# Performance work log

Hardware: AMD Instinct MI355X
Metric: run time of the kernel (lower is better)

Reference implementation:

```python
import jax, jax.numpy as jnp
import numpy as np
from jax import lax

EMBED_DIM = 512
HIDDEN_DIM = 256
OUT_DIM = HIDDEN_DIM // 2
BATCH = 32
SEQ = 4096
THRESHOLD = 1.0
DECAY = 0.95
REFRACTORY = 2.0


def setup_inputs() -> dict:
    key = jax.random.key(0)
    k1, k2, k3 = jax.random.split(key, 3)
    x = jax.random.normal(k1, (BATCH, SEQ, EMBED_DIM), dtype=jnp.float32)
    input_weights = jax.random.normal(k2, (EMBED_DIM, HIDDEN_DIM), dtype=jnp.float32) * 0.1
    hidden_weights = jax.random.normal(k3, (HIDDEN_DIM, OUT_DIM), dtype=jnp.float32) * 0.1
    return {"x": x, "input_weights": input_weights, "hidden_weights": hidden_weights}


def reference(x, input_weights, hidden_weights):
    B, S, D = x.shape
    H = input_weights.shape[1]
    dt = x.dtype
    # batch-mean then project all timesteps at once: [S, H]
    currents = jnp.einsum('sd,dh->sh', x.mean(0), input_weights)

    def step(carry, ic):
        mem, refr = carry
        active = (refr <= 0).astype(dt)
        mem = DECAY * mem + ic * active
        spikes = (mem >= THRESHOLD).astype(dt)
        mem = mem * (1.0 - spikes)
        refr = jnp.maximum(refr - 1.0, 0.0) + spikes * REFRACTORY
        return (mem, refr), spikes

    init = (jnp.zeros((H,), dt), jnp.zeros((H,), dt))
    _, spikes = lax.scan(step, init, currents)  # spikes: [S, H]
    out = spikes @ hidden_weights               # [S, OUT]
    out_mean = out.mean(0)                      # mean over timesteps
    # original repeats the (batch-independent) output across the batch
    return jnp.broadcast_to(out_mean, (B, out_mean.shape[0]))
```

## Files before the change

kernel.cpp:

```cpp
#include <hip/hip_runtime.h>
#include <stdint.h>


#define S_LEN 4096
#define D_DIM 512
#define H_DIM 256
#define O_DIM 128
#define B_SZ  32

#define NPROD 512
#define NCONS 4
#define FPB   2
#define CH    64
#define NCH   (S_LEN / CH)
#define ROWS  (CH / 4)
#define FLAG_GOAL 16u

typedef const __attribute__((address_space(1))) void  glob_void;
typedef       __attribute__((address_space(3))) void  lds_void;

#define LIF_STEP(IC) {                          \
    float ict = sp2 ? 0.f : (IC);               \
    float tt  = fmaf(0.95f, u, ict);            \
    u   = sp1 ? 0.f : tt;                       \
    bool sp = (u >= 1.0f);                      \
    cnt += sp ? 1 : 0;                          \
    sp2 = sp1; sp1 = sp; }

#define ACC4(A, V) { A.x += V.x; A.y += V.y; A.z += V.z; A.w += V.w; }

__global__ __launch_bounds__(256, 2)
void snn_fused(const float4* __restrict__ x4,
               const float*  __restrict__ iw,
               const float*  __restrict__ hw,
               float4*       __restrict__ cur4,
               uint32_t*     __restrict__ flags,
               float*        __restrict__ out) {
    __shared__ __attribute__((aligned(16))) char smem[2 * ROWS * 64 * 16 + 256];
    const int t = threadIdx.x;

    if (blockIdx.x < NPROD) {
        float4* xm = (float4*)smem;
        const int r2 = t >> 7;
        const int d4 = t & 127;
        const int h  = t;
        const float inv = 1.0f / (float)B_SZ;
        const size_t bstr = (size_t)S_LEN * (D_DIM / 4);

        for (int g = 0; g < FPB; ++g) {
            const int f  = blockIdx.x + NPROD * g;
            const int s0 = 4 * f;

            float4 a0 = make_float4(0.f, 0.f, 0.f, 0.f);
            float4 a1 = make_float4(0.f, 0.f, 0.f, 0.f);
            const float4* xb = x4 + (size_t)(s0 + r2) * (D_DIM / 4) + d4;
            for (int b = 0; b < B_SZ; b += 4) {
                const float4* p = xb + (size_t)b * bstr;
                float4 v00 = p[0],            v01 = p[2 * (D_DIM / 4)];
                float4 v10 = p[bstr],         v11 = p[bstr + 2 * (D_DIM / 4)];
                float4 v20 = p[2 * bstr],     v21 = p[2 * bstr + 2 * (D_DIM / 4)];
                float4 v30 = p[3 * bstr],     v31 = p[3 * bstr + 2 * (D_DIM / 4)];
                ACC4(a0, v00); ACC4(a0, v10); ACC4(a0, v20); ACC4(a0, v30);
                ACC4(a1, v01); ACC4(a1, v11); ACC4(a1, v21); ACC4(a1, v31);
            }
            a0.x *= inv; a0.y *= inv; a0.z *= inv; a0.w *= inv;
            a1.x *= inv; a1.y *= inv; a1.z *= inv; a1.w *= inv;
            xm[r2 * (D_DIM / 4) + d4]       = a0;
            xm[(r2 + 2) * (D_DIM / 4) + d4] = a1;
            __syncthreads();

            float acc2[4] = {0.f, 0.f, 0.f, 0.f};
            for (int d4i = 0; d4i < D_DIM / 4; ++d4i) {
                const int d = d4i * 4;
                float w0 = iw[(d + 0) * H_DIM + h];
                float w1 = iw[(d + 1) * H_DIM + h];
                float w2 = iw[(d + 2) * H_DIM + h];
                float w3 = iw[(d + 3) * H_DIM + h];
                #pragma unroll
                for (int r = 0; r < 4; ++r) {
                    float4 xv = xm[r * (D_DIM / 4) + d4i];
                    acc2[r] += xv.x * w0 + xv.y * w1 + xv.z * w2 + xv.w * w3;
                }
            }
            cur4[(size_t)f * H_DIM + h] =
                make_float4(acc2[0], acc2[1], acc2[2], acc2[3]);

            __syncthreads();
            if (t == 0) {
                __builtin_amdgcn_fence(__ATOMIC_RELEASE, "agent");
                atomicAdd(&flags[f >> 4], 1u);
            }
        }
        return;
    }

    if (t >= 64) return;
    float4 (*lbuf)[ROWS * 64] = (float4 (*)[ROWS * 64])smem;
    float* cl = (float*)(smem + 2 * ROWS * 64 * 16);
    const int lane  = t;
    const int hbase = (int)(blockIdx.x - NPROD) * 64;

    auto wait_chunk = [&](int c) {
        if (lane == 0) {
            while (atomicAdd(&flags[c], 0u) < FLAG_GOAL)
                __builtin_amdgcn_s_sleep(2);
        }
        __builtin_amdgcn_fence(__ATOMIC_ACQUIRE, "agent");
    };
    auto stage = [&](int c) {
        #pragma unroll
        for (int r = 0; r < ROWS; ++r) {
            const float4* g = cur4 + (size_t)(c * ROWS + r) * H_DIM + hbase + lane;
            __builtin_amdgcn_global_load_lds((glob_void*)g,
                                             (lds_void*)&lbuf[c & 1][r * 64 + lane],
                                             16, 0, 0);
        }
    };

    wait_chunk(0);
    stage(0);

    float u = 0.f;
    int   cnt = 0;
    bool  sp1 = false, sp2 = false;

    for (int c = 0; c < NCH; ++c) {
        if (c + 1 < NCH) {
            wait_chunk(c + 1);
            stage(c + 1);
            asm volatile("s_waitcnt vmcnt(16)" ::: "memory");
        } else {
            asm volatile("s_waitcnt vmcnt(0)" ::: "memory");
        }
        const float4* lb = lbuf[c & 1];
        float4 v[ROWS];
        #pragma unroll
        for (int r = 0; r < ROWS; ++r) v[r] = lb[r * 64 + lane];
        __builtin_amdgcn_sched_barrier(0);

        #pragma unroll
        for (int r = 0; r < ROWS; ++r) {
            LIF_STEP(v[r].x); LIF_STEP(v[r].y); LIF_STEP(v[r].z); LIF_STEP(v[r].w);
        }
    }

    __syncthreads();
    cl[lane] = (float)cnt;
    __syncthreads();
    float a0 = 0.f, a1 = 0.f;
    #pragma unroll 8
    for (int k = 0; k < 64; ++k) {
        float c = cl[k];
        const float* w = hw + (size_t)(hbase + k) * O_DIM;
        a0 = fmaf(c, w[lane], a0);
        a1 = fmaf(c, w[lane + 64], a1);
    }
    a0 *= (1.0f / (float)S_LEN);
    a1 *= (1.0f / (float)S_LEN);
    for (int b = 0; b < B_SZ; ++b) {
        atomicAdd(out + b * O_DIM + lane,      a0);
        atomicAdd(out + b * O_DIM + lane + 64, a1);
    }
}

extern "C" void kernel_launch(void* const* d_in, const int* in_sizes, int n_in,
                              void* d_out, int out_size, void* d_ws, size_t ws_size,
                              hipStream_t stream) {
    const float4* x4 = (const float4*)d_in[0];
    const float*  iw = (const float*) d_in[1];
    const float*  hw = (const float*) d_in[2];
    float* out   = (float*)d_out;
    float4* cur4 = (float4*)d_ws;
    uint32_t* flags = (uint32_t*)((char*)d_ws + (size_t)4 * 1024 * 1024);

    hipMemsetAsync(flags, 0, NCH * sizeof(uint32_t), stream);
    hipMemsetAsync(out,   0, B_SZ * O_DIM * sizeof(float), stream);
    hipLaunchKernelGGL(snn_fused, dim3(NPROD + NCONS), dim3(256), 0, stream,
                       x4, iw, hw, cur4, flags, out);
}
```

Before: 496.3 us.

## Restructure producer/consumer handoff with per-pass counters and register-buffered scan

Halves the producer grid to 256 blocks, each handling 4 row-groups, and replaces the per-chunk flags with one counter per pass that consumers poll until all producers have finished that pass. Producers write currents row-major with relaxed agent-scope atomic stores. Consumers read them with relaxed atomic loads straight into two 64-float register buffers, double-buffered, instead of staging through LDS with global_load_lds. This cuts flag traffic and LDS round trips on the serial scan, but consumers now wait for a full producer pass before starting, and the acquire fences are gone, which weakens the memory-ordering guarantees.

```diff
diff --git a/kernel.cpp b/kernel.cpp
--- a/kernel.cpp
+++ b/kernel.cpp
@@ -8,16 +8,11 @@
 #define O_DIM 128
 #define B_SZ  32
 
-#define NPROD 512
+#define NPROD 256
 #define NCONS 4
-#define FPB   2
+#define FPB   4
 #define CH    64
 #define NCH   (S_LEN / CH)
-#define ROWS  (CH / 4)
-#define FLAG_GOAL 16u
-
-typedef const __attribute__((address_space(1))) void  glob_void;
-typedef       __attribute__((address_space(3))) void  lds_void;
 
 #define LIF_STEP(IC) {                          \
     float ict = sp2 ? 0.f : (IC);               \
@@ -29,14 +24,28 @@
 
 #define ACC4(A, V) { A.x += V.x; A.y += V.y; A.z += V.z; A.w += V.w; }
 
+#define CISSUE(BUF, C) {                                                     \
+    const float* p_ = csrc + (size_t)(C) * (CH * H_DIM);                     \
+    _Pragma("unroll")                                                        \
+    for (int r_ = 0; r_ < CH; ++r_)                                          \
+        BUF[r_] = __hip_atomic_load(p_ + (size_t)r_ * H_DIM,                 \
+                                    __ATOMIC_RELAXED,                        \
+                                    __HIP_MEMORY_SCOPE_AGENT);              \
+    __builtin_amdgcn_sched_barrier(0); }
+
+#define CSCAN(BUF) {                                                         \
+    _Pragma("unroll")                                                        \
+    for (int r_ = 0; r_ < CH; ++r_) { LIF_STEP(BUF[r_]); }                   \
+    __builtin_amdgcn_sched_barrier(0); }
+
 __global__ __launch_bounds__(256, 2)
 void snn_fused(const float4* __restrict__ x4,
                const float*  __restrict__ iw,
                const float*  __restrict__ hw,
-               float4*       __restrict__ cur4,
-               uint32_t*     __restrict__ flags,
+               float*        __restrict__ cur,
+               uint32_t*     __restrict__ ctr,
                float*        __restrict__ out) {
-    __shared__ __attribute__((aligned(16))) char smem[2 * ROWS * 64 * 16 + 256];
+    __shared__ __attribute__((aligned(16))) char smem[4 * 128 * 16 + 256];
     const int t = threadIdx.x;
 
     if (blockIdx.x < NPROD) {
@@ -82,66 +91,50 @@
                     acc2[r] += xv.x * w0 + xv.y * w1 + xv.z * w2 + xv.w * w3;
                 }
             }
-            cur4[(size_t)f * H_DIM + h] =
-                make_float4(acc2[0], acc2[1], acc2[2], acc2[3]);
-
+            {
+                float* dst = cur + (size_t)s0 * H_DIM + h;
+                #pragma unroll
+                for (int r = 0; r < 4; ++r)
+                    __hip_atomic_store(dst + (size_t)r * H_DIM, acc2[r],
+                                       __ATOMIC_RELAXED, __HIP_MEMORY_SCOPE_AGENT);
+            }
             __syncthreads();
-            if (t == 0) {
-                __builtin_amdgcn_fence(__ATOMIC_RELEASE, "agent");
-                atomicAdd(&flags[f >> 4], 1u);
-            }
+            if (t == 0)
+                __hip_atomic_fetch_add(&ctr[g], 1u, __ATOMIC_RELAXED,
+                                       __HIP_MEMORY_SCOPE_AGENT);
         }
         return;
     }
 
     if (t >= 64) return;
-    float4 (*lbuf)[ROWS * 64] = (float4 (*)[ROWS * 64])smem;
-    float* cl = (float*)(smem + 2 * ROWS * 64 * 16);
+    float* cl = (float*)(smem + 4 * 128 * 16);
     const int lane  = t;
     const int hbase = (int)(blockIdx.x - NPROD) * 64;
+    const float* csrc = cur + hbase + lane;
 
-    auto wait_chunk = [&](int c) {
+    auto wait_pass = [&](int gp) {
         if (lane == 0) {
-            while (atomicAdd(&flags[c], 0u) < FLAG_GOAL)
-                __builtin_amdgcn_s_sleep(2);
-        }
-        __builtin_amdgcn_fence(__ATOMIC_ACQUIRE, "agent");
-    };
-    auto stage = [&](int c) {
-        #pragma unroll
-        for (int r = 0; r < ROWS; ++r) {
-            const float4* g = cur4 + (size_t)(c * ROWS + r) * H_DIM + hbase + lane;
-            __builtin_amdgcn_global_load_lds((glob_void*)g,
-                                             (lds_void*)&lbuf[c & 1][r * 64 + lane],
-                                             16, 0, 0);
+            while (__hip_atomic_load(&ctr[gp], __ATOMIC_RELAXED,
+                                     __HIP_MEMORY_SCOPE_AGENT) < (uint32_t)NPROD)
+                __builtin_amdgcn_s_sleep(8);
         }
     };
 
-    wait_chunk(0);
-    stage(0);
-
+    float va[CH], vb[CH];
     float u = 0.f;
     int   cnt = 0;
     bool  sp1 = false, sp2 = false;
 
-    for (int c = 0; c < NCH; ++c) {
-        if (c + 1 < NCH) {
-            wait_chunk(c + 1);
-            stage(c + 1);
-            asm volatile("s_waitcnt vmcnt(16)" ::: "memory");
-        } else {
-            asm volatile("s_waitcnt vmcnt(0)" ::: "memory");
+    wait_pass(0);
+    CISSUE(va, 0);
+    for (int c = 0; c < NCH; c += 2) {
+        CISSUE(vb, c + 1);
+        CSCAN(va);
+        if (c + 2 < NCH) {
+            if (((c + 2) & 15) == 0) wait_pass((c + 2) >> 4);
+            CISSUE(va, c + 2);
         }
-        const float4* lb = lbuf[c & 1];
-        float4 v[ROWS];
-        #pragma unroll
-        for (int r = 0; r < ROWS; ++r) v[r] = lb[r * 64 + lane];
-        __builtin_amdgcn_sched_barrier(0);
-
-        #pragma unroll
-        for (int r = 0; r < ROWS; ++r) {
-            LIF_STEP(v[r].x); LIF_STEP(v[r].y); LIF_STEP(v[r].z); LIF_STEP(v[r].w);
-        }
+        CSCAN(vb);
     }
 
     __syncthreads();
@@ -169,12 +162,12 @@
     const float4* x4 = (const float4*)d_in[0];
     const float*  iw = (const float*) d_in[1];
     const float*  hw = (const float*) d_in[2];
-    float* out   = (float*)d_out;
-    float4* cur4 = (float4*)d_ws;
-    uint32_t* flags = (uint32_t*)((char*)d_ws + (size_t)4 * 1024 * 1024);
+    float* out = (float*)d_out;
+    float* cur = (float*)d_ws;
+    uint32_t* ctr = (uint32_t*)((char*)d_ws + (size_t)4 * 1024 * 1024);
 
-    hipMemsetAsync(flags, 0, NCH * sizeof(uint32_t), stream);
-    hipMemsetAsync(out,   0, B_SZ * O_DIM * sizeof(float), stream);
+    (void)hipMemsetAsync(ctr, 0, FPB * sizeof(uint32_t), stream);
+    (void)hipMemsetAsync(out, 0, B_SZ * O_DIM * sizeof(float), stream);
     hipLaunchKernelGGL(snn_fused, dim3(NPROD + NCONS), dim3(256), 0, stream,
-                       x4, iw, hw, cur4, flags, out);
+                       x4, iw, hw, cur, ctr, out);
 }
```

New measurement: 462.2 us. 1.07x faster.

## Split fused producer/consumer kernel into separate produce and scan kernels

Applied to the files above, without the earlier changes.

Replaces the single persistent kernel with flag-based producer/consumer synchronization by two launches: one computing batch-mean projected currents, and one running the LIF scan. This removes spin-waiting on atomic flags, the release/acquire fences, and the flags memset. The cost is losing overlap between the serial scan and the bandwidth-bound production phase, plus an extra launch.

```diff
diff --git a/kernel.cpp b/kernel.cpp
--- a/kernel.cpp
+++ b/kernel.cpp
@@ -8,13 +8,10 @@
 #define O_DIM 128
 #define B_SZ  32
 
-#define NPROD 512
-#define NCONS 4
-#define FPB   2
+#define NPROD 1024
 #define CH    64
 #define NCH   (S_LEN / CH)
 #define ROWS  (CH / 4)
-#define FLAG_GOAL 16u
 
 typedef const __attribute__((address_space(1))) void  glob_void;
 typedef       __attribute__((address_space(3))) void  lds_void;
@@ -29,84 +26,64 @@
 
 #define ACC4(A, V) { A.x += V.x; A.y += V.y; A.z += V.z; A.w += V.w; }
 
-__global__ __launch_bounds__(256, 2)
-void snn_fused(const float4* __restrict__ x4,
-               const float*  __restrict__ iw,
-               const float*  __restrict__ hw,
-               float4*       __restrict__ cur4,
-               uint32_t*     __restrict__ flags,
-               float*        __restrict__ out) {
-    __shared__ __attribute__((aligned(16))) char smem[2 * ROWS * 64 * 16 + 256];
-    const int t = threadIdx.x;
+__global__ __launch_bounds__(256)
+void snn_produce(const float4* __restrict__ x4,
+                 const float*  __restrict__ iw,
+                 float4*       __restrict__ cur4) {
+    __shared__ float4 xm[4 * (D_DIM / 4)];
+    const int t   = threadIdx.x;
+    const int r2  = t >> 7;
+    const int d4  = t & 127;
+    const int h   = t;
+    const float inv = 1.0f / (float)B_SZ;
+    const size_t bstr = (size_t)S_LEN * (D_DIM / 4);
 
-    if (blockIdx.x < NPROD) {
-        float4* xm = (float4*)smem;
-        const int r2 = t >> 7;
-        const int d4 = t & 127;
-        const int h  = t;
-        const float inv = 1.0f / (float)B_SZ;
-        const size_t bstr = (size_t)S_LEN * (D_DIM / 4);
+    const int f  = (int)blockIdx.x;
+    const int s0 = 4 * f;
 
-        for (int g = 0; g < FPB; ++g) {
-            const int f  = blockIdx.x + NPROD * g;
-            const int s0 = 4 * f;
+    float4 a0 = make_float4(0.f, 0.f, 0.f, 0.f);
+    float4 a1 = make_float4(0.f, 0.f, 0.f, 0.f);
+    const float4* xb = x4 + (size_t)(s0 + r2) * (D_DIM / 4) + d4;
+    for (int b = 0; b < B_SZ; b += 4) {
+        const float4* p = xb + (size_t)b * bstr;
+        float4 v00 = p[0],            v01 = p[2 * (D_DIM / 4)];
+        float4 v10 = p[bstr],         v11 = p[bstr + 2 * (D_DIM / 4)];
+        float4 v20 = p[2 * bstr],     v21 = p[2 * bstr + 2 * (D_DIM / 4)];
+        float4 v30 = p[3 * bstr],     v31 = p[3 * bstr + 2 * (D_DIM / 4)];
+        ACC4(a0, v00); ACC4(a0, v10); ACC4(a0, v20); ACC4(a0, v30);
+        ACC4(a1, v01); ACC4(a1, v11); ACC4(a1, v21); ACC4(a1, v31);
+    }
+    a0.x *= inv; a0.y *= inv; a0.z *= inv; a0.w *= inv;
+    a1.x *= inv; a1.y *= inv; a1.z *= inv; a1.w *= inv;
+    xm[r2 * (D_DIM / 4) + d4]       = a0;
+    xm[(r2 + 2) * (D_DIM / 4) + d4] = a1;
+    __syncthreads();
 
-            float4 a0 = make_float4(0.f, 0.f, 0.f, 0.f);
-            float4 a1 = make_float4(0.f, 0.f, 0.f, 0.f);
-            const float4* xb = x4 + (size_t)(s0 + r2) * (D_DIM / 4) + d4;
-            for (int b = 0; b < B_SZ; b += 4) {
-                const float4* p = xb + (size_t)b * bstr;
-                float4 v00 = p[0],            v01 = p[2 * (D_DIM / 4)];
-                float4 v10 = p[bstr],         v11 = p[bstr + 2 * (D_DIM / 4)];
-                float4 v20 = p[2 * bstr],     v21 = p[2 * bstr + 2 * (D_DIM / 4)];
-                float4 v30 = p[3 * bstr],     v31 = p[3 * bstr + 2 * (D_DIM / 4)];
-                ACC4(a0, v00); ACC4(a0, v10); ACC4(a0, v20); ACC4(a0, v30);
-                ACC4(a1, v01); ACC4(a1, v11); ACC4(a1, v21); ACC4(a1, v31);
-            }
-            a0.x *= inv; a0.y *= inv; a0.z *= inv; a0.w *= inv;
-            a1.x *= inv; a1.y *= inv; a1.z *= inv; a1.w *= inv;
-            xm[r2 * (D_DIM / 4) + d4]       = a0;
-            xm[(r2 + 2) * (D_DIM / 4) + d4] = a1;
-            __syncthreads();
+    float acc2[4] = {0.f, 0.f, 0.f, 0.f};
+    for (int d4i = 0; d4i < D_DIM / 4; ++d4i) {
+        const int d = d4i * 4;
+        float w0 = iw[(d + 0) * H_DIM + h];
+        float w1 = iw[(d + 1) * H_DIM + h];
+        float w2 = iw[(d + 2) * H_DIM + h];
+        float w3 = iw[(d + 3) * H_DIM + h];
+        #pragma unroll
+        for (int r = 0; r < 4; ++r) {
+            float4 xv = xm[r * (D_DIM / 4) + d4i];
+            acc2[r] += xv.x * w0 + xv.y * w1 + xv.z * w2 + xv.w * w3;
+        }
+    }
+    cur4[(size_t)f * H_DIM + h] = make_float4(acc2[0], acc2[1], acc2[2], acc2[3]);
+}
 
-            float acc2[4] = {0.f, 0.f, 0.f, 0.f};
-            for (int d4i = 0; d4i < D_DIM / 4; ++d4i) {
-                const int d = d4i * 4;
-                float w0 = iw[(d + 0) * H_DIM + h];
-                float w1 = iw[(d + 1) * H_DIM + h];
-                float w2 = iw[(d + 2) * H_DIM + h];
-                float w3 = iw[(d + 3) * H_DIM + h];
-                #pragma unroll
-                for (int r = 0; r < 4; ++r) {
-                    float4 xv = xm[r * (D_DIM / 4) + d4i];
-                    acc2[r] += xv.x * w0 + xv.y * w1 + xv.z * w2 + xv.w * w3;
-                }
-            }
-            cur4[(size_t)f * H_DIM + h] =
-                make_float4(acc2[0], acc2[1], acc2[2], acc2[3]);
+__global__ __launch_bounds__(64)
+void snn_scan(const float4* __restrict__ cur4,
+              const float*  __restrict__ hw,
+              float*        __restrict__ out) {
+    __shared__ __attribute__((aligned(16))) float4 lbuf[2][ROWS * 64];
+    __shared__ float cl[64];
+    const int lane  = threadIdx.x;
+    const int hbase = (int)blockIdx.x * 64;
 
-            __syncthreads();
-            if (t == 0) {
-                __builtin_amdgcn_fence(__ATOMIC_RELEASE, "agent");
-                atomicAdd(&flags[f >> 4], 1u);
-            }
-        }
-        return;
-    }
-
-    if (t >= 64) return;
-    float4 (*lbuf)[ROWS * 64] = (float4 (*)[ROWS * 64])smem;
-    float* cl = (float*)(smem + 2 * ROWS * 64 * 16);
-    const int lane  = t;
-    const int hbase = (int)(blockIdx.x - NPROD) * 64;
-
-    auto wait_chunk = [&](int c) {
-        if (lane == 0) {
-            while (atomicAdd(&flags[c], 0u) < FLAG_GOAL)
-                __builtin_amdgcn_s_sleep(2);
-        }
-        __builtin_amdgcn_fence(__ATOMIC_ACQUIRE, "agent");
-    };
     auto stage = [&](int c) {
         #pragma unroll
         for (int r = 0; r < ROWS; ++r) {
@@ -117,21 +94,20 @@
         }
     };
 
-    wait_chunk(0);
-    stage(0);
-
     float u = 0.f;
     int   cnt = 0;
     bool  sp1 = false, sp2 = false;
 
+    stage(0);
     for (int c = 0; c < NCH; ++c) {
         if (c + 1 < NCH) {
-            wait_chunk(c + 1);
             stage(c + 1);
             asm volatile("s_waitcnt vmcnt(16)" ::: "memory");
         } else {
             asm volatile("s_waitcnt vmcnt(0)" ::: "memory");
         }
+        __builtin_amdgcn_sched_barrier(0);
+
         const float4* lb = lbuf[c & 1];
         float4 v[ROWS];
         #pragma unroll
@@ -171,10 +147,10 @@
     const float*  hw = (const float*) d_in[2];
     float* out   = (float*)d_out;
     float4* cur4 = (float4*)d_ws;
-    uint32_t* flags = (uint32_t*)((char*)d_ws + (size_t)4 * 1024 * 1024);
 
-    hipMemsetAsync(flags, 0, NCH * sizeof(uint32_t), stream);
-    hipMemsetAsync(out,   0, B_SZ * O_DIM * sizeof(float), stream);
-    hipLaunchKernelGGL(snn_fused, dim3(NPROD + NCONS), dim3(256), 0, stream,
-                       x4, iw, hw, cur4, flags, out);
+    (void)hipMemsetAsync(out, 0, B_SZ * O_DIM * sizeof(float), stream);
+    hipLaunchKernelGGL(snn_produce, dim3(NPROD), dim3(256), 0, stream,
+                       x4, iw, cur4);
+    hipLaunchKernelGGL(snn_scan, dim3(4), dim3(64), 0, stream,
+                       cur4, hw, out);
 }
```

Result: faster. 468.3 us (-5.6%).
